# Optimization experiments

Hardware: AMD Instinct MI355X
Metric: run time of the kernel (lower is better)

## Reference

```python
import jax, jax.numpy as jnp
import numpy as np

N, D_IN, D_OUT, C = 4096, 512, 16384, 256
THRESHOLD = 0.01
TEMPERATURE = 0.1


def setup_inputs() -> dict:
    key = jax.random.key(0)
    k1, k2, k3, k4, k5 = jax.random.split(key, 5)
    inp = jax.random.normal(k1, (N, D_IN), dtype=jnp.float32)
    # kaiming_uniform(a=sqrt(5)) ~ U(-1/sqrt(fan_in), 1/sqrt(fan_in)) scale
    bound = 1.0 / np.sqrt(D_IN)
    weight = jax.random.uniform(k2, (D_OUT, D_IN), minval=-bound, maxval=bound, dtype=jnp.float32)
    bias = jax.random.uniform(k3, (D_OUT,), minval=-bound, maxval=bound, dtype=jnp.float32)
    centroids = jax.random.normal(k4, (C, D_IN), dtype=jnp.float32) * bound
    # disjoint partition of output rows into clusters (stand-in for kmeans labels)
    assignment = jax.random.randint(k5, (D_OUT,), 0, C, dtype=jnp.int32)
    return {"input": inp, "weight": weight, "bias": bias,
            "centroids": centroids, "assignment": assignment}


def reference(input, weight, bias, centroids, assignment):
    # routing: softmax over centroid similarities, threshold
    dots = jax.nn.softmax((input @ centroids.T) / TEMPERATURE, axis=-1)  # [N, C]
    active = dots > THRESHOLD                                            # [N, C] bool
    # torch.unique(query_indices) -> queries active for ANY cluster
    qmask = jnp.any(active, axis=1)                                      # [N]
    # torch.unique(cluster_indices) -> clusters active for ANY query (global union)
    cmask = jnp.any(active, axis=0)                                      # [C]
    # concat(unpad(indices[top_clusters])) -> output rows in any active cluster
    row_mask = cmask[assignment]                                         # [D_OUT]
    # out[top_q].index_copy(1, top_rows, linear(...)); rest stays zero
    dense = input @ weight.T + bias                                      # [N, D_OUT]
    out = dense * qmask[:, None].astype(dense.dtype) * row_mask[None, :].astype(dense.dtype)
    return out
```

## Files before the change

### kernel.cpp

```cpp
#include <hip/hip_runtime.h>
#include <stdint.h>

#define N_Q    4096
#define D_K    512
#define D_OUT  16384
#define NCLUST 256

#define BM 128
#define BN 128
#define BK 32
#define NT (D_K / BK)
#define SCP 132

typedef __attribute__((ext_vector_type(4))) float f32x4;
typedef __attribute__((ext_vector_type(8))) short bf16x8;

__device__ __forceinline__ uint32_t f2bf(float f) {
  uint32_t u = __float_as_uint(f);
  u += 0x7FFFu + ((u >> 16) & 1u);
  return u >> 16;
}

#define GLOAD_LDS16(g, l)                                         \
  __builtin_amdgcn_global_load_lds(                               \
      (const __attribute__((address_space(1))) void*)(g),         \
      (__attribute__((address_space(3))) void*)(l), 16, 0, 0)

#define WAIT_BAR(N) asm volatile("s_waitcnt vmcnt(" #N ")\n\ts_barrier" ::: "memory")
#define LBAR() asm volatile("s_waitcnt lgkmcnt(0)\n\ts_barrier" ::: "memory")

__global__ __launch_bounds__(256) void prep_kernel(const float* __restrict__ weight,
                                                   ushort* __restrict__ W_bf,
                                                   const float* __restrict__ cent,
                                                   float4* __restrict__ centT4,
                                                   float* __restrict__ cmask) {
  int b = blockIdx.x;
  if (b < (D_OUT * D_K / 8) / 256) {
    int i = b * 256 + threadIdx.x;
    const float4* s = reinterpret_cast<const float4*>(weight) + (size_t)i * 2;
    float4 v0 = s[0], v1 = s[1];
    uint4 o;
    o.x = f2bf(v0.x) | (f2bf(v0.y) << 16);
    o.y = f2bf(v0.z) | (f2bf(v0.w) << 16);
    o.z = f2bf(v1.x) | (f2bf(v1.y) << 16);
    o.w = f2bf(v1.z) | (f2bf(v1.w) << 16);
    reinterpret_cast<uint4*>(W_bf)[i] = o;
  } else {
    int bb = b - (D_OUT * D_K / 8) / 256;
    if (bb == 0) cmask[threadIdx.x] = 0.0f;
    int idx = bb * 256 + threadIdx.x;
    int k4 = idx & 127, c = idx >> 7;
    float4 v = *reinterpret_cast<const float4*>(&cent[(size_t)c * D_K + k4 * 4]);
    centT4[(size_t)k4 * NCLUST + c] = v;
  }
}

__global__ __launch_bounds__(256) void routing_kernel(const float* __restrict__ input,
                                                      const float4* __restrict__ centT4,
                                                      float* __restrict__ qmask,
                                                      float* __restrict__ cmask,
                                                      ushort* __restrict__ A_bf) {
  __shared__ float lgs[8][NCLUST];
  int c = threadIdx.x;
  int q0 = blockIdx.x * 8;
  const float* __restrict__ inp = input + (size_t)q0 * D_K;

  {
    const float4* s4 = reinterpret_cast<const float4*>(inp) + c * 4;
    float4 x0 = s4[0], x1 = s4[1], x2 = s4[2], x3 = s4[3];
    uint4 o0, o1;
    o0.x = f2bf(x0.x) | (f2bf(x0.y) << 16);
    o0.y = f2bf(x0.z) | (f2bf(x0.w) << 16);
    o0.z = f2bf(x1.x) | (f2bf(x1.y) << 16);
    o0.w = f2bf(x1.z) | (f2bf(x1.w) << 16);
    o1.x = f2bf(x2.x) | (f2bf(x2.y) << 16);
    o1.y = f2bf(x2.z) | (f2bf(x2.w) << 16);
    o1.z = f2bf(x3.x) | (f2bf(x3.y) << 16);
    o1.w = f2bf(x3.z) | (f2bf(x3.w) << 16);
    uint4* dst = reinterpret_cast<uint4*>(A_bf + (size_t)q0 * D_K);
    dst[c * 2] = o0;
    dst[c * 2 + 1] = o1;
  }

  float acc[8] = {0, 0, 0, 0, 0, 0, 0, 0};
  for (int k4 = 0; k4 < D_K / 4; ++k4) {
    float4 v = centT4[(size_t)k4 * NCLUST + c];
#pragma unroll
    for (int q = 0; q < 8; ++q) {
      float4 r = *reinterpret_cast<const float4*>(&inp[q * D_K + k4 * 4]);
      acc[q] += v.x * r.x + v.y * r.y + v.z * r.z + v.w * r.w;
    }
  }
#pragma unroll
  for (int q = 0; q < 8; ++q) lgs[q][c] = acc[q] * 10.0f;
  __syncthreads();

  int wave = c >> 6, lane = c & 63;
#pragma unroll
  for (int qq = 0; qq < 2; ++qq) {
    int q = wave * 2 + qq;
    float4 lv = *reinterpret_cast<const float4*>(&lgs[q][lane * 4]);
    float m = fmaxf(fmaxf(lv.x, lv.y), fmaxf(lv.z, lv.w));
#pragma unroll
    for (int off = 32; off > 0; off >>= 1) m = fmaxf(m, __shfl_xor(m, off));
    float e0 = expf(lv.x - m), e1 = expf(lv.y - m), e2 = expf(lv.z - m), e3 = expf(lv.w - m);
    float s = e0 + e1 + e2 + e3;
#pragma unroll
    for (int off = 32; off > 0; off >>= 1) s += __shfl_xor(s, off);
    float thr = 0.01f * s;
    bool a0 = e0 > thr, a1 = e1 > thr, a2 = e2 > thr, a3 = e3 > thr;
    if (a0) cmask[lane * 4 + 0] = 1.0f;
    if (a1) cmask[lane * 4 + 1] = 1.0f;
    if (a2) cmask[lane * 4 + 2] = 1.0f;
    if (a3) cmask[lane * 4 + 3] = 1.0f;
    unsigned long long any = __ballot(a0 | a1 | a2 | a3);
    if (lane == 0) qmask[q0 + q] = any ? 1.0f : 0.0f;
  }
}

__global__ __launch_bounds__(256, 3) void gemm_masked_kernel(
    const ushort* __restrict__ A, const ushort* __restrict__ W,
    const float* __restrict__ bias, const int* __restrict__ assign,
    const float* __restrict__ qmask, const float* __restrict__ cmask,
    float* __restrict__ C) {
  __shared__ __align__(16) char smem[49152];

  int tid = threadIdx.x;
  int wave = tid >> 6, lane = tid & 63;

  int bid = blockIdx.x;
  int idx = bid >> 3;
  int ntile = (bid & 7) * 16 + (idx & 15);
  int mtile = idx >> 4;
  int m0 = mtile * BM, n0 = ntile * BN;

  int wr = wave >> 1, wc = wave & 1;

  int srow = tid >> 2, kg = tid & 3;
  int ks = (kg ^ ((srow >> 1) & 3)) * 8;
  const ushort* srcA0 = A + (size_t)(m0 + srow) * D_K + ks;
  const ushort* srcA1 = srcA0 + (size_t)64 * D_K;
  const ushort* srcB0 = W + (size_t)(n0 + srow) * D_K + ks;
  const ushort* srcB1 = srcB0 + (size_t)64 * D_K;
  int wo = wave << 10;

#define STAGE(j) do {                                    \
    char* sl_ = smem + ((j) % 3) * 16384 + wo;           \
    GLOAD_LDS16(srcA0 + (j) * BK, sl_);                  \
    GLOAD_LDS16(srcA1 + (j) * BK, sl_ + 4096);           \
    GLOAD_LDS16(srcB0 + (j) * BK, sl_ + 8192);           \
    GLOAD_LDS16(srcB1 + (j) * BK, sl_ + 12288);          \
  } while (0)

  int kg0 = lane >> 4, l15 = lane & 15, lr = lane >> 4;
  int aIdx[4], bIdx[4];
#pragma unroll
  for (int m = 0; m < 4; ++m) {
    int r = wr * 64 + m * 16 + l15;
    aIdx[m] = r * 32 + ((kg0 ^ ((r >> 1) & 3)) << 3);
  }
#pragma unroll
  for (int n = 0; n < 4; ++n) {
    int r = wc * 64 + n * 16 + l15;
    bIdx[n] = 4096 + r * 32 + ((kg0 ^ ((r >> 1) & 3)) << 3);
  }

  f32x4 acc[4][4] = {};

  STAGE(0);
  STAGE(1);

#pragma unroll
  for (int t = 0; t < NT; ++t) {
    if (t < NT - 1) { WAIT_BAR(4); } else { WAIT_BAR(0); }

    const ushort* sl = (const ushort*)(smem + (t % 3) * 16384);
    bf16x8 af[4], bf[4];
#pragma unroll
    for (int n = 0; n < 4; ++n) bf[n] = *reinterpret_cast<const bf16x8*>(&sl[bIdx[n]]);
#pragma unroll
    for (int m = 0; m < 4; ++m) af[m] = *reinterpret_cast<const bf16x8*>(&sl[aIdx[m]]);
    if (t + 2 < NT) STAGE(t + 2);

    __builtin_amdgcn_s_setprio(1);
#pragma unroll
    for (int m = 0; m < 4; ++m)
#pragma unroll
      for (int n = 0; n < 4; ++n)
        acc[m][n] = __builtin_amdgcn_mfma_f32_16x16x32_bf16(af[m], bf[n], acc[m][n], 0, 0, 0);
    __builtin_amdgcn_s_setprio(0);
  }
#undef STAGE

  LBAR();

  float* sC = reinterpret_cast<float*>(smem);
  float bj[4], rm[4];
#pragma unroll
  for (int n = 0; n < 4; ++n) {
    int col = n0 + wc * 64 + n * 16 + l15;
    bj[n] = bias[col];
    rm[n] = cmask[assign[col]];
  }
#pragma unroll
  for (int m = 0; m < 4; ++m) {
    float4 qm = *reinterpret_cast<const float4*>(&qmask[m0 + wr * 64 + m * 16 + lr * 4]);
    int rl = wr * 16 + lr * 4;
#pragma unroll
    for (int n = 0; n < 4; ++n) {
      int cc = wc * 64 + n * 16 + l15;
      sC[(rl + 0) * SCP + cc] = (acc[m][n][0] + bj[n]) * qm.x * rm[n];
      sC[(rl + 1) * SCP + cc] = (acc[m][n][1] + bj[n]) * qm.y * rm[n];
      sC[(rl + 2) * SCP + cc] = (acc[m][n][2] + bj[n]) * qm.z * rm[n];
      sC[(rl + 3) * SCP + cc] = (acc[m][n][3] + bj[n]) * qm.w * rm[n];
    }
    LBAR();
    f32x4 v[4];
#pragma unroll
    for (int i = 0; i < 4; ++i) {
      int s = wave * 8 + i * 2 + (lane >> 5);
      v[i] = *reinterpret_cast<const f32x4*>(&sC[s * SCP + (lane & 31) * 4]);
    }
    LBAR();
#pragma unroll
    for (int i = 0; i < 4; ++i) {
      int s = wave * 8 + i * 2 + (lane >> 5);
      int grow = m0 + (s >> 4) * 64 + m * 16 + (s & 15);
      __builtin_nontemporal_store(
          v[i], reinterpret_cast<f32x4*>(&C[(size_t)grow * D_OUT + n0 + (lane & 31) * 4]));
    }
  }
}

extern "C" void kernel_launch(void* const* d_in, const int* in_sizes, int n_in,
                              void* d_out, int out_size, void* d_ws, size_t ws_size,
                              hipStream_t stream) {
  const float* input     = (const float*)d_in[0];
  const float* weight    = (const float*)d_in[1];
  const float* bias      = (const float*)d_in[2];
  const float* centroids = (const float*)d_in[3];
  const int*   assign    = (const int*)d_in[4];
  float* out = (float*)d_out;

  char* ws = (char*)d_ws;
  ushort* A_bf   = (ushort*)ws;
  ushort* W_bf   = (ushort*)(ws + 4194304);
  float*  qmask  = (float*)(ws + 20971520);
  float*  cmask  = (float*)(ws + 20987904);
  float4* centT4 = (float4*)(ws + 21000192);

  prep_kernel<<<4224, 256, 0, stream>>>(weight, W_bf, centroids, centT4, cmask);
  routing_kernel<<<N_Q / 8, 256, 0, stream>>>(input, centT4, qmask, cmask, A_bf);
  gemm_masked_kernel<<<(N_Q / BM) * (D_OUT / BN), 256, 0, stream>>>(
      A_bf, W_bf, bias, assign, qmask, cmask, out);
}
```

Baseline: 133.1 us.

## Load A operand directly from global into registers, stage only W in LDS

Removes LDS staging for the activation (A) tile. Each wave now prefetches its own A fragments one k-step ahead with inline-asm global_load_dwordx4, while the weight tile keeps its triple-buffered global-to-LDS path. This halves the LDS footprint and cuts the LDS reads for A. The cost is that waves sharing the same rows fetch A twice from global/L2. Correctness now depends on hand-tuned vmcnt counts, since the compiler cannot track the asm loads.

```diff
diff --git a/kernel.cpp b/kernel.cpp
--- a/kernel.cpp
+++ b/kernel.cpp
@@ -26,8 +26,18 @@
       (const __attribute__((address_space(1))) void*)(g),         \
       (__attribute__((address_space(3))) void*)(l), 16, 0, 0)
 
-#define WAIT_BAR(N) asm volatile("s_waitcnt vmcnt(" #N ")\n\ts_barrier" ::: "memory")
+__device__ __forceinline__ bf16x8 gload16(const ushort* p) {
+  bf16x8 r;
+  asm volatile("global_load_dwordx4 %0, %1, off" : "=v"(r) : "v"(p));
+  return r;
+}
+
+#define WAIT_BAR(N) do {                                                   \
+    asm volatile("s_waitcnt vmcnt(" #N ")\n\ts_barrier" ::: "memory");     \
+    __builtin_amdgcn_sched_barrier(0);                                     \
+  } while (0)
 #define LBAR() asm volatile("s_waitcnt lgkmcnt(0)\n\ts_barrier" ::: "memory")
+#define CFENCE() asm volatile("" ::: "memory")
 
 __global__ __launch_bounds__(256) void prep_kernel(const float* __restrict__ weight,
                                                    ushort* __restrict__ W_bf,
@@ -123,7 +133,7 @@
     const float* __restrict__ bias, const int* __restrict__ assign,
     const float* __restrict__ qmask, const float* __restrict__ cmask,
     float* __restrict__ C) {
-  __shared__ __align__(16) char smem[49152];
+  __shared__ __align__(16) char smem[24576];
 
   int tid = threadIdx.x;
   int wave = tid >> 6, lane = tid & 63;
@@ -138,57 +148,65 @@
 
   int srow = tid >> 2, kg = tid & 3;
   int ks = (kg ^ ((srow >> 1) & 3)) * 8;
-  const ushort* srcA0 = A + (size_t)(m0 + srow) * D_K + ks;
-  const ushort* srcA1 = srcA0 + (size_t)64 * D_K;
   const ushort* srcB0 = W + (size_t)(n0 + srow) * D_K + ks;
   const ushort* srcB1 = srcB0 + (size_t)64 * D_K;
   int wo = wave << 10;
 
 #define STAGE(j) do {                                    \
-    char* sl_ = smem + ((j) % 3) * 16384 + wo;           \
-    GLOAD_LDS16(srcA0 + (j) * BK, sl_);                  \
-    GLOAD_LDS16(srcA1 + (j) * BK, sl_ + 4096);           \
-    GLOAD_LDS16(srcB0 + (j) * BK, sl_ + 8192);           \
-    GLOAD_LDS16(srcB1 + (j) * BK, sl_ + 12288);          \
+    char* sl_ = smem + ((j) % 3) * 8192 + wo;            \
+    GLOAD_LDS16(srcB0 + (j) * BK, sl_);                  \
+    GLOAD_LDS16(srcB1 + (j) * BK, sl_ + 4096);           \
   } while (0)
 
   int kg0 = lane >> 4, l15 = lane & 15, lr = lane >> 4;
-  int aIdx[4], bIdx[4];
-#pragma unroll
-  for (int m = 0; m < 4; ++m) {
-    int r = wr * 64 + m * 16 + l15;
-    aIdx[m] = r * 32 + ((kg0 ^ ((r >> 1) & 3)) << 3);
-  }
+  int bIdx[4];
 #pragma unroll
   for (int n = 0; n < 4; ++n) {
     int r = wc * 64 + n * 16 + l15;
-    bIdx[n] = 4096 + r * 32 + ((kg0 ^ ((r >> 1) & 3)) << 3);
-  }
+    bIdx[n] = r * 32 + ((kg0 ^ ((r >> 1) & 3)) << 3);
+  }
+  const ushort* pA[4];
+#pragma unroll
+  for (int m = 0; m < 4; ++m)
+    pA[m] = A + (size_t)(m0 + wr * 64 + m * 16 + l15) * D_K + kg0 * 8;
 
   f32x4 acc[4][4] = {};
 
   STAGE(0);
   STAGE(1);
+  bf16x8 ac[4];
+#pragma unroll
+  for (int m = 0; m < 4; ++m) ac[m] = gload16(pA[m]);
 
 #pragma unroll
   for (int t = 0; t < NT; ++t) {
-    if (t < NT - 1) { WAIT_BAR(4); } else { WAIT_BAR(0); }
-
-    const ushort* sl = (const ushort*)(smem + (t % 3) * 16384);
-    bf16x8 af[4], bf[4];
-#pragma unroll
-    for (int n = 0; n < 4; ++n) bf[n] = *reinterpret_cast<const bf16x8*>(&sl[bIdx[n]]);
-#pragma unroll
-    for (int m = 0; m < 4; ++m) af[m] = *reinterpret_cast<const bf16x8*>(&sl[aIdx[m]]);
+    if (t == 0 || t == NT - 1) { WAIT_BAR(0); } else { WAIT_BAR(2); }
+
+    bf16x8 an[4];
+    if (t + 1 < NT) {
+#pragma unroll
+      for (int m = 0; m < 4; ++m) an[m] = gload16(pA[m] + (t + 1) * BK);
+      CFENCE();
+    }
     if (t + 2 < NT) STAGE(t + 2);
 
+    const ushort* sb = (const ushort*)(smem + (t % 3) * 8192);
+    bf16x8 bf[4];
+#pragma unroll
+    for (int n = 0; n < 4; ++n) bf[n] = *reinterpret_cast<const bf16x8*>(&sb[bIdx[n]]);
+
     __builtin_amdgcn_s_setprio(1);
 #pragma unroll
     for (int m = 0; m < 4; ++m)
 #pragma unroll
       for (int n = 0; n < 4; ++n)
-        acc[m][n] = __builtin_amdgcn_mfma_f32_16x16x32_bf16(af[m], bf[n], acc[m][n], 0, 0, 0);
+        acc[m][n] = __builtin_amdgcn_mfma_f32_16x16x32_bf16(ac[m], bf[n], acc[m][n], 0, 0, 0);
     __builtin_amdgcn_s_setprio(0);
+
+    if (t + 1 < NT) {
+#pragma unroll
+      for (int m = 0; m < 4; ++m) ac[m] = an[m];
+    }
   }
 #undef STAGE
 
```

Measured after the change: 195.4 us. 1.47x slower.
